# Kernel tuning notes

Measured on AMD Instinct MI355X. Metric: run time of the kernel, lower is better.

Reference implementation:

```python
import jax, jax.numpy as jnp
import numpy as np

B, C, H, W = 16, 128, 128, 128
CO = C // 2  # conv output channels


def _binary_activation(x):
    # forward: sign(x); backward: piecewise-polynomial surrogate (STE)
    out_fwd = jnp.sign(x)
    m1 = (x < -1).astype(x.dtype)
    m2 = (x < 0).astype(x.dtype)
    m3 = (x < 1).astype(x.dtype)
    out1 = -1.0 * m1 + (x * x + 2.0 * x) * (1.0 - m1)
    out2 = out1 * m2 + (-x * x + 2.0 * x) * (1.0 - m2)
    out3 = out2 * m3 + 1.0 * (1.0 - m3)
    return jax.lax.stop_gradient(out_fwd) - jax.lax.stop_gradient(out3) + out3


def _binary_weights(conv_w):
    w = conv_w.reshape(CO, C, 3, 3)
    # per-output-channel mean(|w|), detached
    sf = jax.lax.stop_gradient(jnp.mean(jnp.abs(w), axis=(1, 2, 3), keepdims=True))
    bw_ng = sf * jnp.sign(w)
    wc = jnp.clip(w, -1.0, 1.0)
    return jax.lax.stop_gradient(bw_ng) - jax.lax.stop_gradient(wc) + wc


def setup_inputs() -> dict:
    key = jax.random.key(0)
    k1, k2, k3 = jax.random.split(key, 3)
    x = jax.random.normal(k1, (B, C, H, W), dtype=jnp.float32)
    bias1 = jnp.zeros((1, C, 1, 1), dtype=jnp.float32)
    prelu_a = jnp.full((1, C, 1, 1), 0.25, dtype=jnp.float32)
    bias2 = jnp.zeros((1, C, 1, 1), dtype=jnp.float32)
    # stored flat like HardBinaryConv.weights; zero-mean so signs are mixed
    conv_w = jax.random.normal(k2, (CO * C * 9, 1), dtype=jnp.float32) * 0.001
    # grouped 1x1 conv: groups=CO, 2 input channels per group
    pool_w = jax.random.normal(k3, (CO, 2, 1, 1), dtype=jnp.float32) * 0.1
    return {"x": x, "bias1": bias1, "prelu_a": prelu_a, "bias2": bias2,
            "conv_w": conv_w, "pool_w": pool_w}


def reference(x, bias1, prelu_a, bias2, conv_w, pool_w):
    b, c, h, w = x.shape
    co = c // 2
    out = x + bias1
    out = jnp.maximum(out, 0.0) + prelu_a * jnp.minimum(out, 0.0)  # PReLU per-channel
    out = out + bias2
    out = _binary_activation(out)
    bw = _binary_weights(conv_w)
    y = jax.lax.conv_general_dilated(out, bw, window_strides=(1, 1),
                                     padding=((1, 1), (1, 1)),
                                     dimension_numbers=("NCHW", "OIHW", "NCHW"))
    # grouped 1x1 channel pool: out chan o = w[o,0]*x[2o] + w[o,1]*x[2o+1]
    shortcut = jnp.sum(x.reshape(b, co, 2, h, w) * pool_w.reshape(1, co, 2, 1, 1), axis=2)
    y = y + shortcut
    # PixelUnshuffle(2): (B,co,H,W) -> (B,4*co,H/2,W/2)
    ho, wo = h // 2, w // 2
    y = y.reshape(b, co, ho, 2, wo, 2).transpose(0, 1, 3, 5, 2, 4).reshape(b, co * 4, ho, wo)
    return y
```

## Files before the change

### kernel.cpp

```cpp
#include <hip/hip_runtime.h>
#include <stdint.h>

typedef __attribute__((ext_vector_type(4))) float f32x4;
typedef __attribute__((ext_vector_type(4))) unsigned int u32x4;
typedef __attribute__((ext_vector_type(4))) int i32x4;

#define NB 16
#define NC 128
#define NH 128
#define NW 128
#define WP 130

__device__ __forceinline__ int swz7(int wp) { return (wp ^ (wp >> 3)) & 7; }

__global__ __launch_bounds__(256) void k_prep(const float* __restrict__ cw,
                                              const float* __restrict__ b1,
                                              const float* __restrict__ pa,
                                              const float* __restrict__ b2,
                                              float* __restrict__ sf,
                                              float* __restrict__ theta,
                                              unsigned char* __restrict__ wf) {
    int b = blockIdx.x, t = threadIdx.x;
    int f = b * 256 + t;
    int bb  = f & 15;
    int l   = (f >> 4) & 63;
    int ni  = (f >> 10) & 3;
    int m   = (f >> 12) & 1;
    int p   = f >> 13;
    int o = ni * 16 + (l & 15);
    int c = m * 64 + (l >> 4) * 16 + bb;
    float wv = cw[o * 1152 + c * 9 + p];
    wf[f] = wv > 0.f ? (unsigned char)0x01
                     : (wv < 0.f ? (unsigned char)0xFF : (unsigned char)0x00);
    if (b < 64) {
        __shared__ float red[4];
        const float* pp = cw + b * 1152;
        float s = 0.f;
        for (int i = t; i < 1152; i += 256) s += fabsf(pp[i]);
#pragma unroll
        for (int off = 32; off > 0; off >>= 1) s += __shfl_down(s, off);
        if ((t & 63) == 0) red[t >> 6] = s;
        __syncthreads();
        if (t == 0) sf[b] = (red[0] + red[1] + red[2] + red[3]) * (1.0f / 1152.0f);
    }
    if (b == 64 && t < NC) {
        float B1 = b1[t], A = pa[t], B2 = b2[t];
        theta[t] = (-B2 >= 0.f) ? (-B1 - B2) : (-B1 - B2 / A);
    }
}

__device__ __forceinline__ unsigned int pki8(float v, float th) {
    return v > th ? 0x01u : (v < th ? 0xFFu : 0u);
}

__global__ __launch_bounds__(256, 2) void k_fused(
    const float* __restrict__ x, const float* __restrict__ theta,
    const float* __restrict__ pw, const unsigned char* __restrict__ wf,
    const float* __restrict__ sf, float* __restrict__ out) {
    __shared__ __align__(16) unsigned char AT[69632];
    int bxr = blockIdx.x;
    int bx = (bxr & 7) * 128 + (bxr >> 3);
    int nb = bx >> 6;
    int h2b = bx & 63;
    int t = threadIdx.x;
    int wid = t >> 6;
    int l = t & 63;
    int lr = l & 15, lg = l >> 4;

    if (t < 64) {
        int rho = t >> 4, side = (t >> 3) & 1, u = t & 7;
        int wp = side ? (WP - 1) : 0;
        u32x4 z = {0u, 0u, 0u, 0u};
        *(u32x4*)(AT + (size_t)(rho * WP + wp) * NC + ((u ^ swz7(wp)) << 4)) = z;
    }

    int w4 = t & 31, cg = t >> 5;
    const float* xbase = x + ((size_t)nb * NC + cg * 16) * (NH * NW) + 4 * w4;
    f32x4 th0 = *(const f32x4*)(theta + cg * 16);
    f32x4 th1 = *(const f32x4*)(theta + cg * 16 + 4);
    f32x4 th2 = *(const f32x4*)(theta + cg * 16 + 8);
    f32x4 th3 = *(const f32x4*)(theta + cg * 16 + 12);
    f32x4 p0 = *(const f32x4*)(pw + cg * 16);
    f32x4 p1 = *(const f32x4*)(pw + cg * 16 + 4);
    f32x4 p2 = *(const f32x4*)(pw + cg * 16 + 8);
    f32x4 p3 = *(const f32x4*)(pw + cg * 16 + 12);
    float pwv[16] = {p0.x, p0.y, p0.z, p0.w, p1.x, p1.y, p1.z, p1.w,
                     p2.x, p2.y, p2.z, p2.w, p3.x, p3.y, p3.z, p3.w};
    float sc0[8][4], sc1[8][4];
    f32x4 XA[16], XB[16], XC[16];

#define ISSUE(XR, HH) \
    { const float* xp = xbase + (size_t)(HH) * NW; \
      _Pragma("unroll") for (int cc = 0; cc < 16; ++cc) \
          XR[cc] = *(const f32x4*)(xp + (size_t)cc * (NH * NW)); }
#define PACKROWM(RHO, XR, EM) \
    _Pragma("unroll") for (int ww = 0; ww < 4; ++ww) { \
        int wp = 4 * w4 + ww + 1; \
        u32x4 v; \
        v.x = (pki8(XR[0][ww], th0.x) | (pki8(XR[1][ww], th0.y) << 8) | \
               (pki8(XR[2][ww], th0.z) << 16) | (pki8(XR[3][ww], th0.w) << 24)) & (EM); \
        v.y = (pki8(XR[4][ww], th1.x) | (pki8(XR[5][ww], th1.y) << 8) | \
               (pki8(XR[6][ww], th1.z) << 16) | (pki8(XR[7][ww], th1.w) << 24)) & (EM); \
        v.z = (pki8(XR[8][ww], th2.x) | (pki8(XR[9][ww], th2.y) << 8) | \
               (pki8(XR[10][ww], th2.z) << 16) | (pki8(XR[11][ww], th2.w) << 24)) & (EM); \
        v.w = (pki8(XR[12][ww], th3.x) | (pki8(XR[13][ww], th3.y) << 8) | \
               (pki8(XR[14][ww], th3.z) << 16) | (pki8(XR[15][ww], th3.w) << 24)) & (EM); \
        *(u32x4*)(AT + (size_t)((RHO) * WP + wp) * NC + ((cg ^ swz7(wp)) << 4)) = v; \
    }
#define SCROW(SC, XR) \
    _Pragma("unroll") for (int i = 0; i < 8; ++i) { \
        float wa = pwv[2 * i], wb = pwv[2 * i + 1]; \
        _Pragma("unroll") for (int ww = 0; ww < 4; ++ww) \
            SC[i][ww] = wa * XR[2 * i][ww] + wb * XR[2 * i + 1][ww]; \
    }

    int hTop = (h2b > 0) ? (2 * h2b - 1) : 0;
    int hBot = (h2b < 63) ? (2 * h2b + 2) : 127;
    unsigned emT = (h2b > 0) ? 0xFFFFFFFFu : 0u;
    unsigned emB = (h2b < 63) ? 0xFFFFFFFFu : 0u;

    ISSUE(XA, hTop)
    ISSUE(XB, 2 * h2b)
    ISSUE(XC, 2 * h2b + 1)
    __builtin_amdgcn_sched_barrier(0);
    PACKROWM(0, XA, emT)
    ISSUE(XA, hBot)
    __builtin_amdgcn_sched_barrier(0);
    PACKROWM(1, XB, 0xFFFFFFFFu)
    SCROW(sc0, XB)
    PACKROWM(2, XC, 0xFFFFFFFFu)
    SCROW(sc1, XC)
    PACKROWM(3, XA, emB)

    float sfr[4];
#pragma unroll
    for (int ni = 0; ni < 4; ++ni) sfr[ni] = sf[ni * 16 + lr];

    int w0 = (wid & 1) * 64;
    i32x4 acc[4][4];
    i32x4 zero = {0, 0, 0, 0};
#pragma unroll
    for (int mi = 0; mi < 4; ++mi)
#pragma unroll
        for (int ni = 0; ni < 4; ++ni) acc[mi][ni] = zero;
    __syncthreads();

    __builtin_amdgcn_s_setprio(1);
#pragma unroll
    for (int p = 0; p < 9; ++p) {
        int kh = p / 3, kw = p % 3;
        int rho = (wid >> 1) + kh;
        int wp = w0 + kw + lr;
        const unsigned char* ap = AT + (size_t)(rho * WP + wp) * NC;
        const unsigned char* brow = wf + p * 8192 + l * 16;
        i32x4 bfr[2][4];
#pragma unroll
        for (int m = 0; m < 2; ++m)
#pragma unroll
            for (int ni = 0; ni < 4; ++ni)
                bfr[m][ni] = *(const i32x4*)(brow + m * 4096 + ni * 1024);
#pragma unroll
        for (int mi = 0; mi < 4; ++mi) {
            int s7m = swz7(wp + mi * 16);
            i32x4 a0 = *(const i32x4*)(ap + mi * 2048 + ((lg ^ s7m) << 4));
            i32x4 a1 = *(const i32x4*)(ap + mi * 2048 + (((lg + 4) ^ s7m) << 4));
#pragma unroll
            for (int ni = 0; ni < 4; ++ni) {
                acc[mi][ni] = __builtin_amdgcn_mfma_i32_16x16x64_i8(
                    a0, bfr[0][ni], acc[mi][ni], 0, 0, 0);
                acc[mi][ni] = __builtin_amdgcn_mfma_i32_16x16x64_i8(
                    a1, bfr[1][ni], acc[mi][ni], 0, 0, 0);
            }
        }
    }
    __builtin_amdgcn_s_setprio(0);
    __syncthreads();

    float (*Tt)[68] = (float (*)[68])(AT + wid * 17408);
#pragma unroll
    for (int mi = 0; mi < 4; ++mi)
#pragma unroll
        for (int ni = 0; ni < 4; ++ni) {
            f32x4 cv;
            cv.x = (float)acc[mi][ni].x * sfr[ni];
            cv.y = (float)acc[mi][ni].y * sfr[ni];
            cv.z = (float)acc[mi][ni].z * sfr[ni];
            cv.w = (float)acc[mi][ni].w * sfr[ni];
            int krow = ((ni * 2 + (lr >> 3)) & 7) << 2;
            *(f32x4*)&Tt[ni * 16 + lr][(mi * 16 + lg * 4) ^ krow] = cv;
        }
    __syncthreads();

    int wha = w4 >> 4, w4l = w4 & 15;
#define EPIROW(R2, SC) { \
    const float (*Ts)[68] = (const float (*)[68])(AT + ((R2) * 2 + wha) * 17408); \
    float* obr = out + (((size_t)nb * 256 + (R2) * 2) * 64 + h2b) * 64 + 2 * w4; \
    _Pragma("unroll") for (int i = 0; i < 8; ++i) { \
        int o = 8 * cg + i; \
        int krd = ((o >> 3) & 7) << 2; \
        f32x4 cv = *(const f32x4*)&Ts[o][(4 * w4l) ^ krd]; \
        float2 A = {cv.x + SC[i][0], cv.z + SC[i][2]}; \
        float2 B = {cv.y + SC[i][1], cv.w + SC[i][3]}; \
        *(float2*)(obr + (size_t)o * 16384)        = A; \
        *(float2*)(obr + (size_t)o * 16384 + 4096) = B; \
    } }
    EPIROW(0, sc0)
    EPIROW(1, sc1)
}

extern "C" void kernel_launch(void* const* d_in, const int* in_sizes, int n_in,
                              void* d_out, int out_size, void* d_ws, size_t ws_size,
                              hipStream_t stream) {
    const float* x  = (const float*)d_in[0];
    const float* b1 = (const float*)d_in[1];
    const float* pa = (const float*)d_in[2];
    const float* b2 = (const float*)d_in[3];
    const float* cw = (const float*)d_in[4];
    const float* pw = (const float*)d_in[5];
    float* out = (float*)d_out;
    float* sf = (float*)d_ws;
    float* theta = (float*)((char*)d_ws + 256);
    unsigned char* wfr = (unsigned char*)d_ws + 768;

    k_prep<<<288, 256, 0, stream>>>(cw, b1, pa, b2, sf, theta, wfr);
    k_fused<<<1024, 256, 0, stream>>>(x, theta, pw, wfr, sf, out);
}
```

Baseline: 72.15 us.

## Double block size to 512 threads, splitting channel groups and MFMA M-tiles

Doubles the threads per block so each thread loads and packs 8 channels instead of 16, and each wave computes half of the M tiles of its row/column slab. The aim is more resident waves per CU, lower register pressure and better latency hiding for the global loads and MFMA work. In exchange, each wave now reloads the full weight fragments, doubling redundant weight traffic, and there are more waves competing at the barriers.

```diff
diff --git a/kernel.cpp b/kernel.cpp
--- a/kernel.cpp
+++ b/kernel.cpp
@@ -53,7 +53,7 @@
     return v > th ? 0x01u : (v < th ? 0xFFu : 0u);
 }
 
-__global__ __launch_bounds__(256, 2) void k_fused(
+__global__ __launch_bounds__(512, 4) void k_fused(
     const float* __restrict__ x, const float* __restrict__ theta,
     const float* __restrict__ pw, const unsigned char* __restrict__ wf,
     const float* __restrict__ sf, float* __restrict__ out) {
@@ -75,41 +75,33 @@
     }
 
     int w4 = t & 31, cg = t >> 5;
-    const float* xbase = x + ((size_t)nb * NC + cg * 16) * (NH * NW) + 4 * w4;
-    f32x4 th0 = *(const f32x4*)(theta + cg * 16);
-    f32x4 th1 = *(const f32x4*)(theta + cg * 16 + 4);
-    f32x4 th2 = *(const f32x4*)(theta + cg * 16 + 8);
-    f32x4 th3 = *(const f32x4*)(theta + cg * 16 + 12);
-    f32x4 p0 = *(const f32x4*)(pw + cg * 16);
-    f32x4 p1 = *(const f32x4*)(pw + cg * 16 + 4);
-    f32x4 p2 = *(const f32x4*)(pw + cg * 16 + 8);
-    f32x4 p3 = *(const f32x4*)(pw + cg * 16 + 12);
-    float pwv[16] = {p0.x, p0.y, p0.z, p0.w, p1.x, p1.y, p1.z, p1.w,
-                     p2.x, p2.y, p2.z, p2.w, p3.x, p3.y, p3.z, p3.w};
-    float sc0[8][4], sc1[8][4];
-    f32x4 XA[16], XB[16], XC[16];
+    int uu = cg >> 1, half = cg & 1;
+    const float* xbase = x + ((size_t)nb * NC + cg * 8) * (NH * NW) + 4 * w4;
+    f32x4 th0 = *(const f32x4*)(theta + cg * 8);
+    f32x4 th1 = *(const f32x4*)(theta + cg * 8 + 4);
+    f32x4 pw0 = *(const f32x4*)(pw + cg * 8);
+    f32x4 pw1 = *(const f32x4*)(pw + cg * 8 + 4);
+    float pwf[8] = {pw0.x, pw0.y, pw0.z, pw0.w, pw1.x, pw1.y, pw1.z, pw1.w};
+    float sc0[4][4], sc1[4][4];
+    f32x4 XA[8], XB[8], XC[8];
 
 #define ISSUE(XR, HH) \
     { const float* xp = xbase + (size_t)(HH) * NW; \
-      _Pragma("unroll") for (int cc = 0; cc < 16; ++cc) \
+      _Pragma("unroll") for (int cc = 0; cc < 8; ++cc) \
           XR[cc] = *(const f32x4*)(xp + (size_t)cc * (NH * NW)); }
 #define PACKROWM(RHO, XR, EM) \
     _Pragma("unroll") for (int ww = 0; ww < 4; ++ww) { \
         int wp = 4 * w4 + ww + 1; \
-        u32x4 v; \
+        uint2 v; \
         v.x = (pki8(XR[0][ww], th0.x) | (pki8(XR[1][ww], th0.y) << 8) | \
                (pki8(XR[2][ww], th0.z) << 16) | (pki8(XR[3][ww], th0.w) << 24)) & (EM); \
         v.y = (pki8(XR[4][ww], th1.x) | (pki8(XR[5][ww], th1.y) << 8) | \
                (pki8(XR[6][ww], th1.z) << 16) | (pki8(XR[7][ww], th1.w) << 24)) & (EM); \
-        v.z = (pki8(XR[8][ww], th2.x) | (pki8(XR[9][ww], th2.y) << 8) | \
-               (pki8(XR[10][ww], th2.z) << 16) | (pki8(XR[11][ww], th2.w) << 24)) & (EM); \
-        v.w = (pki8(XR[12][ww], th3.x) | (pki8(XR[13][ww], th3.y) << 8) | \
-               (pki8(XR[14][ww], th3.z) << 16) | (pki8(XR[15][ww], th3.w) << 24)) & (EM); \
-        *(u32x4*)(AT + (size_t)((RHO) * WP + wp) * NC + ((cg ^ swz7(wp)) << 4)) = v; \
+        *(uint2*)(AT + (size_t)((RHO) * WP + wp) * NC + ((uu ^ swz7(wp)) << 4) + half * 8) = v; \
     }
 #define SCROW(SC, XR) \
-    _Pragma("unroll") for (int i = 0; i < 8; ++i) { \
-        float wa = pwv[2 * i], wb = pwv[2 * i + 1]; \
+    _Pragma("unroll") for (int i = 0; i < 4; ++i) { \
+        float wa = pwf[2 * i], wb = pwf[2 * i + 1]; \
         _Pragma("unroll") for (int ww = 0; ww < 4; ++ww) \
             SC[i][ww] = wa * XR[2 * i][ww] + wb * XR[2 * i + 1][ww]; \
     }
@@ -136,11 +128,14 @@
 #pragma unroll
     for (int ni = 0; ni < 4; ++ni) sfr[ni] = sf[ni * 16 + lr];
 
-    int w0 = (wid & 1) * 64;
-    i32x4 acc[4][4];
+    int row = wid >> 2;
+    int ch64 = (wid >> 1) & 1;
+    int mh = wid & 1;
+    int w0 = ch64 * 64;
+    i32x4 acc[2][4];
     i32x4 zero = {0, 0, 0, 0};
 #pragma unroll
-    for (int mi = 0; mi < 4; ++mi)
+    for (int mi = 0; mi < 2; ++mi)
 #pragma unroll
         for (int ni = 0; ni < 4; ++ni) acc[mi][ni] = zero;
     __syncthreads();
@@ -149,7 +144,7 @@
 #pragma unroll
     for (int p = 0; p < 9; ++p) {
         int kh = p / 3, kw = p % 3;
-        int rho = (wid >> 1) + kh;
+        int rho = row + kh;
         int wp = w0 + kw + lr;
         const unsigned char* ap = AT + (size_t)(rho * WP + wp) * NC;
         const unsigned char* brow = wf + p * 8192 + l * 16;
@@ -160,10 +155,11 @@
             for (int ni = 0; ni < 4; ++ni)
                 bfr[m][ni] = *(const i32x4*)(brow + m * 4096 + ni * 1024);
 #pragma unroll
-        for (int mi = 0; mi < 4; ++mi) {
-            int s7m = swz7(wp + mi * 16);
-            i32x4 a0 = *(const i32x4*)(ap + mi * 2048 + ((lg ^ s7m) << 4));
-            i32x4 a1 = *(const i32x4*)(ap + mi * 2048 + (((lg + 4) ^ s7m) << 4));
+        for (int mi = 0; mi < 2; ++mi) {
+            int mig = 2 * mh + mi;
+            int s7m = swz7(wp + mig * 16);
+            i32x4 a0 = *(const i32x4*)(ap + mig * 2048 + ((lg ^ s7m) << 4));
+            i32x4 a1 = *(const i32x4*)(ap + mig * 2048 + (((lg + 4) ^ s7m) << 4));
 #pragma unroll
             for (int ni = 0; ni < 4; ++ni) {
                 acc[mi][ni] = __builtin_amdgcn_mfma_i32_16x16x64_i8(
@@ -176,9 +172,9 @@
     __builtin_amdgcn_s_setprio(0);
     __syncthreads();
 
-    float (*Tt)[68] = (float (*)[68])(AT + wid * 17408);
-#pragma unroll
-    for (int mi = 0; mi < 4; ++mi)
+    float (*Tt)[68] = (float (*)[68])(AT + (wid >> 1) * 17408);
+#pragma unroll
+    for (int mi = 0; mi < 2; ++mi)
 #pragma unroll
         for (int ni = 0; ni < 4; ++ni) {
             f32x4 cv;
@@ -186,8 +182,9 @@
             cv.y = (float)acc[mi][ni].y * sfr[ni];
             cv.z = (float)acc[mi][ni].z * sfr[ni];
             cv.w = (float)acc[mi][ni].w * sfr[ni];
+            int colb = (2 * mh + mi) * 16 + lg * 4;
             int krow = ((ni * 2 + (lr >> 3)) & 7) << 2;
-            *(f32x4*)&Tt[ni * 16 + lr][(mi * 16 + lg * 4) ^ krow] = cv;
+            *(f32x4*)&Tt[ni * 16 + lr][colb ^ krow] = cv;
         }
     __syncthreads();
 
@@ -195,8 +192,8 @@
 #define EPIROW(R2, SC) { \
     const float (*Ts)[68] = (const float (*)[68])(AT + ((R2) * 2 + wha) * 17408); \
     float* obr = out + (((size_t)nb * 256 + (R2) * 2) * 64 + h2b) * 64 + 2 * w4; \
-    _Pragma("unroll") for (int i = 0; i < 8; ++i) { \
-        int o = 8 * cg + i; \
+    _Pragma("unroll") for (int i = 0; i < 4; ++i) { \
+        int o = 4 * cg + i; \
         int krd = ((o >> 3) & 7) << 2; \
         f32x4 cv = *(const f32x4*)&Ts[o][(4 * w4l) ^ krd]; \
         float2 A = {cv.x + SC[i][0], cv.z + SC[i][2]}; \
@@ -223,5 +220,5 @@
     unsigned char* wfr = (unsigned char*)d_ws + 768;
 
     k_prep<<<288, 256, 0, stream>>>(cw, b1, pa, b2, sf, theta, wfr);
-    k_fused<<<1024, 256, 0, stream>>>(x, theta, pw, wfr, sf, out);
-}
+    k_fused<<<1024, 512, 0, stream>>>(x, theta, pw, wfr, sf, out);
+}
```

Result: slower. 112.7 us (+56.2%).

## Shrink fused conv tile to one output row per block for higher occupancy

Applied to the files above, without the earlier changes.

Each block now computes a single output row instead of two. The launch grows to 2048 blocks, LDS drops to about 49 KB, and launch bounds move to 3 blocks per CU. Each wave handles 32 columns with half the accumulators, and the epilogue transpose buffer shrinks to match. The aim is more concurrent blocks and less register/LDS pressure, but every input row is now loaded 3 times instead of 2 (halo overhead), so global read traffic rises.

```diff
diff --git a/kernel.cpp b/kernel.cpp
--- a/kernel.cpp
+++ b/kernel.cpp
@@ -53,21 +53,21 @@
     return v > th ? 0x01u : (v < th ? 0xFFu : 0u);
 }
 
-__global__ __launch_bounds__(256, 2) void k_fused(
+__global__ __launch_bounds__(256, 3) void k_fused(
     const float* __restrict__ x, const float* __restrict__ theta,
     const float* __restrict__ pw, const unsigned char* __restrict__ wf,
     const float* __restrict__ sf, float* __restrict__ out) {
-    __shared__ __align__(16) unsigned char AT[69632];
+    __shared__ __align__(16) unsigned char AT[49920];
     int bxr = blockIdx.x;
-    int bx = (bxr & 7) * 128 + (bxr >> 3);
-    int nb = bx >> 6;
-    int h2b = bx & 63;
+    int bx = (bxr & 7) * 256 + (bxr >> 3);
+    int nb = bx >> 7;
+    int h  = bx & 127;
     int t = threadIdx.x;
     int wid = t >> 6;
     int l = t & 63;
     int lr = l & 15, lg = l >> 4;
 
-    if (t < 64) {
+    if (t < 48) {
         int rho = t >> 4, side = (t >> 3) & 1, u = t & 7;
         int wp = side ? (WP - 1) : 0;
         u32x4 z = {0u, 0u, 0u, 0u};
@@ -86,7 +86,7 @@
     f32x4 p3 = *(const f32x4*)(pw + cg * 16 + 12);
     float pwv[16] = {p0.x, p0.y, p0.z, p0.w, p1.x, p1.y, p1.z, p1.w,
                      p2.x, p2.y, p2.z, p2.w, p3.x, p3.y, p3.z, p3.w};
-    float sc0[8][4], sc1[8][4];
+    float sc[8][4];
     f32x4 XA[16], XB[16], XC[16];
 
 #define ISSUE(XR, HH) \
@@ -107,40 +107,36 @@
                (pki8(XR[14][ww], th3.z) << 16) | (pki8(XR[15][ww], th3.w) << 24)) & (EM); \
         *(u32x4*)(AT + (size_t)((RHO) * WP + wp) * NC + ((cg ^ swz7(wp)) << 4)) = v; \
     }
-#define SCROW(SC, XR) \
-    _Pragma("unroll") for (int i = 0; i < 8; ++i) { \
-        float wa = pwv[2 * i], wb = pwv[2 * i + 1]; \
-        _Pragma("unroll") for (int ww = 0; ww < 4; ++ww) \
-            SC[i][ww] = wa * XR[2 * i][ww] + wb * XR[2 * i + 1][ww]; \
-    }
-
-    int hTop = (h2b > 0) ? (2 * h2b - 1) : 0;
-    int hBot = (h2b < 63) ? (2 * h2b + 2) : 127;
-    unsigned emT = (h2b > 0) ? 0xFFFFFFFFu : 0u;
-    unsigned emB = (h2b < 63) ? 0xFFFFFFFFu : 0u;
+
+    int hTop = (h > 0) ? (h - 1) : 0;
+    int hBot = (h < 127) ? (h + 1) : 127;
+    unsigned emT = (h > 0) ? 0xFFFFFFFFu : 0u;
+    unsigned emB = (h < 127) ? 0xFFFFFFFFu : 0u;
 
     ISSUE(XA, hTop)
-    ISSUE(XB, 2 * h2b)
-    ISSUE(XC, 2 * h2b + 1)
+    ISSUE(XB, h)
+    ISSUE(XC, hBot)
     __builtin_amdgcn_sched_barrier(0);
     PACKROWM(0, XA, emT)
-    ISSUE(XA, hBot)
-    __builtin_amdgcn_sched_barrier(0);
     PACKROWM(1, XB, 0xFFFFFFFFu)
-    SCROW(sc0, XB)
-    PACKROWM(2, XC, 0xFFFFFFFFu)
-    SCROW(sc1, XC)
-    PACKROWM(3, XA, emB)
+#pragma unroll
+    for (int i = 0; i < 8; ++i) {
+        float wa = pwv[2 * i], wb = pwv[2 * i + 1];
+#pragma unroll
+        for (int ww = 0; ww < 4; ++ww)
+            sc[i][ww] = wa * XB[2 * i][ww] + wb * XB[2 * i + 1][ww];
+    }
+    PACKROWM(2, XC, emB)
 
     float sfr[4];
 #pragma unroll
     for (int ni = 0; ni < 4; ++ni) sfr[ni] = sf[ni * 16 + lr];
 
-    int w0 = (wid & 1) * 64;
-    i32x4 acc[4][4];
+    int w0 = wid * 32;
+    i32x4 acc[2][4];
     i32x4 zero = {0, 0, 0, 0};
 #pragma unroll
-    for (int mi = 0; mi < 4; ++mi)
+    for (int mi = 0; mi < 2; ++mi)
 #pragma unroll
         for (int ni = 0; ni < 4; ++ni) acc[mi][ni] = zero;
     __syncthreads();
@@ -149,9 +145,8 @@
 #pragma unroll
     for (int p = 0; p < 9; ++p) {
         int kh = p / 3, kw = p % 3;
-        int rho = (wid >> 1) + kh;
         int wp = w0 + kw + lr;
-        const unsigned char* ap = AT + (size_t)(rho * WP + wp) * NC;
+        const unsigned char* ap = AT + (size_t)(kh * WP + wp) * NC;
         const unsigned char* brow = wf + p * 8192 + l * 16;
         i32x4 bfr[2][4];
 #pragma unroll
@@ -160,7 +155,7 @@
             for (int ni = 0; ni < 4; ++ni)
                 bfr[m][ni] = *(const i32x4*)(brow + m * 4096 + ni * 1024);
 #pragma unroll
-        for (int mi = 0; mi < 4; ++mi) {
+        for (int mi = 0; mi < 2; ++mi) {
             int s7m = swz7(wp + mi * 16);
             i32x4 a0 = *(const i32x4*)(ap + mi * 2048 + ((lg ^ s7m) << 4));
             i32x4 a1 = *(const i32x4*)(ap + mi * 2048 + (((lg + 4) ^ s7m) << 4));
@@ -176,9 +171,9 @@
     __builtin_amdgcn_s_setprio(0);
     __syncthreads();
 
-    float (*Tt)[68] = (float (*)[68])(AT + wid * 17408);
-#pragma unroll
-    for (int mi = 0; mi < 4; ++mi)
+    float (*Tt)[36] = (float (*)[36])(AT + wid * 9216);
+#pragma unroll
+    for (int mi = 0; mi < 2; ++mi)
 #pragma unroll
         for (int ni = 0; ni < 4; ++ni) {
             f32x4 cv;
@@ -186,26 +181,26 @@
             cv.y = (float)acc[mi][ni].y * sfr[ni];
             cv.z = (float)acc[mi][ni].z * sfr[ni];
             cv.w = (float)acc[mi][ni].w * sfr[ni];
+            int colb = mi * 16 + lg * 4;
             int krow = ((ni * 2 + (lr >> 3)) & 7) << 2;
-            *(f32x4*)&Tt[ni * 16 + lr][(mi * 16 + lg * 4) ^ krow] = cv;
+            *(f32x4*)&Tt[ni * 16 + lr][colb ^ krow] = cv;
         }
     __syncthreads();
 
-    int wha = w4 >> 4, w4l = w4 & 15;
-#define EPIROW(R2, SC) { \
-    const float (*Ts)[68] = (const float (*)[68])(AT + ((R2) * 2 + wha) * 17408); \
-    float* obr = out + (((size_t)nb * 256 + (R2) * 2) * 64 + h2b) * 64 + 2 * w4; \
-    _Pragma("unroll") for (int i = 0; i < 8; ++i) { \
-        int o = 8 * cg + i; \
-        int krd = ((o >> 3) & 7) << 2; \
-        f32x4 cv = *(const f32x4*)&Ts[o][(4 * w4l) ^ krd]; \
-        float2 A = {cv.x + SC[i][0], cv.z + SC[i][2]}; \
-        float2 B = {cv.y + SC[i][1], cv.w + SC[i][3]}; \
-        *(float2*)(obr + (size_t)o * 16384)        = A; \
-        *(float2*)(obr + (size_t)o * 16384 + 4096) = B; \
-    } }
-    EPIROW(0, sc0)
-    EPIROW(1, sc1)
+    int wq = w4 >> 3, w4l = w4 & 7;
+    const float (*Ts)[36] = (const float (*)[36])(AT + wq * 9216);
+    int s1 = h & 1, h2 = h >> 1;
+    float* obr = out + (((size_t)nb * 256 + s1 * 2) * 64 + h2) * 64 + 2 * w4;
+#pragma unroll
+    for (int i = 0; i < 8; ++i) {
+        int o = 8 * cg + i;
+        int krd = ((o >> 3) & 7) << 2;
+        f32x4 cv = *(const f32x4*)&Ts[o][(4 * w4l) ^ krd];
+        float2 A = {cv.x + sc[i][0], cv.z + sc[i][2]};
+        float2 B = {cv.y + sc[i][1], cv.w + sc[i][3]};
+        *(float2*)(obr + (size_t)o * 16384)        = A;
+        *(float2*)(obr + (size_t)o * 16384 + 4096) = B;
+    }
 }
 
 extern "C" void kernel_launch(void* const* d_in, const int* in_sizes, int n_in,
@@ -223,5 +218,5 @@
     unsigned char* wfr = (unsigned char*)d_ws + 768;
 
     k_prep<<<288, 256, 0, stream>>>(cw, b1, pa, b2, sf, theta, wfr);
-    k_fused<<<1024, 256, 0, stream>>>(x, theta, pw, wfr, sf, out);
-}
+    k_fused<<<2048, 256, 0, stream>>>(x, theta, pw, wfr, sf, out);
+}
```

Result: slower. 159.0 us (+120.4%).
